# Kernel tuning notes

Measured on AMD Instinct MI355X. Metric: run time of the kernel, lower is better.

## Reference

```python
import jax, jax.numpy as jnp
import numpy as np

TEMP = 0.5
K_SEL = 20
NEG_SLOPE = 0.1


def setup_inputs() -> dict:
    key = jax.random.key(0)
    ks = jax.random.split(key, 12)
    B, N = 64, 20000
    F1, F2, D = 512, 256, 128
    init = lambda k, shape, fan: (jax.random.normal(k, shape) / np.sqrt(fan)).astype(jnp.float32)
    return {
        "patient_embedding": jax.random.normal(ks[0], (B, F1), dtype=jnp.float32),
        "gene_embedding": jax.random.normal(ks[1], (N, F2), dtype=jnp.float32),
        "Wq": init(ks[2], (F1, D), F1), "bq": jnp.zeros((D,), jnp.float32),
        "Wk": init(ks[3], (F2, D), F2), "bk": jnp.zeros((D,), jnp.float32),
        "Wv": init(ks[4], (F2, D), F2), "bv": jnp.zeros((D,), jnp.float32),
        "W1": init(ks[5], (2 * D, D), 2 * D), "b1": jnp.zeros((D,), jnp.float32),
        "w2": init(ks[6], (D,), D), "b2": jnp.zeros((), jnp.float32),
    }


def reference(patient_embedding, gene_embedding, Wq, bq, Wk, bk, Wv, bv, W1, b1, w2, b2):
    B = patient_embedding.shape[0]
    N = gene_embedding.shape[0]
    D = Wq.shape[1]

    Q = patient_embedding @ Wq + bq          # [B, D]
    Km = gene_embedding @ Wk + bk            # [N, D]
    V = gene_embedding @ Wv + bv             # [N, D]

    # MLP attention on cat([Q_exp, K_exp]); split W1 to avoid materializing [B,N,2D]
    q_part = Q @ W1[:D]                      # [B, D]
    k_part = Km @ W1[D:]                     # [N, D]
    h = jax.nn.leaky_relu(q_part[:, None, :] + k_part[None, :, :] + b1, NEG_SLOPE)  # [B, N, D]
    sim = h @ w2 + b2                        # [B, N]
    logits = sim / TEMP

    # gumbel-softmax, hard=True, independent noise per (b, k) row
    g = jax.random.gumbel(jax.random.key(42), (B, K_SEL, N), dtype=logits.dtype)
    y_soft = jax.nn.softmax((logits[:, None, :] + g) / TEMP, axis=-1)   # [B, K, N]
    y_hard = jax.nn.one_hot(jnp.argmax(y_soft, axis=-1), N, dtype=y_soft.dtype)
    masks = y_hard - jax.lax.stop_gradient(y_soft) + y_soft             # straight-through

    topk_values = jnp.einsum("bkn,nd->bkd", masks, V)                   # [B, K, D]
    scores = jnp.einsum("bd,bkd->bk", Q, topk_values) / np.sqrt(D).astype(np.float32)
    weights = jax.nn.softmax(scores, axis=-1)                           # [B, K] (dropout = eval/identity)
    context = jnp.einsum("bk,bkd->bd", weights, topk_values)            # [B, D]
    return context
```

## Files before the change

### kernel.cpp

```cpp
#include <hip/hip_runtime.h>

#define NG 20000
#define BOFF 12800000u

__device__ __forceinline__ void threefry2x32(unsigned x0, unsigned x1,
                                             unsigned& o0, unsigned& o1) {
  const unsigned ks0 = 0u;
  const unsigned ks1 = 42u;
  const unsigned ks2 = 0x1BD11BDAu ^ 0u ^ 42u;
  x0 += ks0; x1 += ks1;
#define TFR(r) { x0 += x1; x1 = (x1 << (r)) | (x1 >> (32 - (r))); x1 ^= x0; }
  TFR(13) TFR(15) TFR(26) TFR(6)
  x0 += ks1; x1 += ks2 + 1u;
  TFR(17) TFR(29) TFR(16) TFR(24)
  x0 += ks2; x1 += ks0 + 2u;
  TFR(13) TFR(15) TFR(26) TFR(6)
  x0 += ks0; x1 += ks1 + 3u;
  TFR(17) TFR(29) TFR(16) TFR(24)
  x0 += ks1; x1 += ks2 + 4u;
  TFR(13) TFR(15) TFR(26) TFR(6)
  x0 += ks2; x1 += ks0 + 5u;
#undef TFR
  o0 = x0; o1 = x1;
}

__device__ __forceinline__ unsigned tfbits(unsigned ctr) {
  unsigned o0, o1;
  threefry2x32(0u, ctr, o0, o1);
  return o0 ^ o1;
}

__device__ __forceinline__ float gumbel32(unsigned bits) {
  float f = __uint_as_float((bits >> 9) | 0x3f800000u) - 1.0f;
  float u = fmaxf(f, 1.17549435e-38f);
  return -__logf(-__logf(u));
}

__device__ __forceinline__ double gumbel64(unsigned bits) {
  float f = __uint_as_float((bits >> 9) | 0x3f800000u) - 1.0f;
  double u = (double)fmaxf(f, 1.17549435e-38f);
  return -log(-log(u));
}

__device__ __forceinline__ unsigned long long packcell(double v, int n) {
  unsigned long long u = (unsigned long long)__double_as_longlong(v);
  u = (u >> 63) ? ~u : (u | 0x8000000000000000ull);
  return (u & 0xFFFFFFFFFFFF8000ull) | (unsigned long long)(32767 - n);
}

__global__ __launch_bounds__(128) void kprep(
    const float* __restrict__ pe, const float* __restrict__ Wq,
    const float* __restrict__ bq, const float* __restrict__ Wk,
    const float* __restrict__ bk, const float* __restrict__ W1,
    const float* __restrict__ b1, const float* __restrict__ w2,
    float* __restrict__ Wf32, double* __restrict__ qbT,
    float* __restrict__ Qm, unsigned long long* __restrict__ cells,
    double2* __restrict__ c12) {
  __shared__ float L[512];
  __shared__ double Ld[128];
  const int t = threadIdx.x;
  const int bid = blockIdx.x;
  if (bid < 256) {
    L[t] = Wk[bid * 128 + t];
    __syncthreads();
    double acc = 0.0;
    #pragma unroll 8
    for (int j = 0; j < 128; ++j)
      acc = fma((double)L[j], (double)W1[(128 + j) * 128 + t], acc);
    Wf32[bid * 128 + t] = (float)acc;
  } else if (bid < 320) {
    const int b = bid - 256;
    #pragma unroll
    for (int i = 0; i < 4; ++i) L[t + 128 * i] = pe[b * 512 + t + 128 * i];
    __syncthreads();
    double q = (double)bq[t];
    #pragma unroll 4
    for (int f = 0; f < 512; ++f)
      q = fma((double)L[f], (double)Wq[f * 128 + t], q);
    Qm[b * 128 + t] = (float)q;
    Ld[t] = q;
    __syncthreads();
    double acc = (double)b1[t];
    #pragma unroll 4
    for (int j = 0; j < 128; ++j) {
      acc = fma(Ld[j], (double)W1[j * 128 + t], acc);
      acc = fma((double)bk[j], (double)W1[(128 + j) * 128 + t], acc);
    }
    qbT[t * 64 + b] = acc;
  } else {
    for (int i = t; i < 1280; i += 128) cells[i] = 0ull;
    const double w2d = (double)w2[t];
    c12[t] = make_double2(0.55 * w2d, 0.45 * w2d);
  }
}

__global__ __launch_bounds__(256) void kfused(
    const float* __restrict__ ge, const float* __restrict__ Wf32,
    const double* __restrict__ qbT, const double2* __restrict__ c12,
    double* __restrict__ simd, float* __restrict__ sim2f) {
  __shared__ double SBd[2048];
  __shared__ float kpL[2048];
  float* geL = (float*)SBd;
  double* simL = SBd;
  const int t = threadIdx.x;
  const int wv = t >> 6;
  const int lane = t & 63;
  const int g0 = blockIdx.x * 16;

  {
    const float4* src = (const float4*)(ge + (size_t)g0 * 256);
    float4* dst = (float4*)geL;
    #pragma unroll
    for (int i = 0; i < 4; ++i) dst[t + i * 256] = src[t + i * 256];
  }
  __syncthreads();

  float acc[4][2];
  #pragma unroll
  for (int j = 0; j < 4; ++j) { acc[j][0] = 0.f; acc[j][1] = 0.f; }
  const float* wb0 = Wf32 + lane;
  const float* wb1 = Wf32 + lane + 64;
  const float* gL = geL + wv * 4 * 256;

  float wc0[4], wc1[4];
  #pragma unroll
  for (int ff = 0; ff < 4; ++ff) {
    wc0[ff] = wb0[ff * 128];
    wc1[ff] = wb1[ff * 128];
  }
  for (int f0 = 0; f0 < 256; f0 += 4) {
    float wn0[4], wn1[4];
    if (f0 < 252) {
      #pragma unroll
      for (int ff = 0; ff < 4; ++ff) {
        wn0[ff] = wb0[(f0 + 4 + ff) * 128];
        wn1[ff] = wb1[(f0 + 4 + ff) * 128];
      }
    }
    #pragma unroll
    for (int j = 0; j < 4; ++j) {
      const float4 gv = *(const float4*)(gL + j * 256 + f0);
      acc[j][0] = fmaf(gv.x, wc0[0], acc[j][0]);
      acc[j][1] = fmaf(gv.x, wc1[0], acc[j][1]);
      acc[j][0] = fmaf(gv.y, wc0[1], acc[j][0]);
      acc[j][1] = fmaf(gv.y, wc1[1], acc[j][1]);
      acc[j][0] = fmaf(gv.z, wc0[2], acc[j][0]);
      acc[j][1] = fmaf(gv.z, wc1[2], acc[j][1]);
      acc[j][0] = fmaf(gv.w, wc0[3], acc[j][0]);
      acc[j][1] = fmaf(gv.w, wc1[3], acc[j][1]);
    }
    #pragma unroll
    for (int ff = 0; ff < 4; ++ff) { wc0[ff] = wn0[ff]; wc1[ff] = wn1[ff]; }
  }

  __syncthreads();
  #pragma unroll
  for (int j = 0; j < 4; ++j) {
    kpL[(wv * 4 + j) * 128 + lane] = acc[j][0];
    kpL[(wv * 4 + j) * 128 + lane + 64] = acc[j][1];
  }
  __syncthreads();

  double s[4];
  #pragma unroll
  for (int j = 0; j < 4; ++j) s[j] = 0.0;
  for (int dd = 0; dd < 128; ++dd) {
    const double2 cc = c12[dd];
    const double qv = qbT[dd * 64 + lane];
    #pragma unroll
    for (int j = 0; j < 4; ++j) {
      const double kv = (double)kpL[(wv + j * 4) * 128 + dd];
      const double tt = qv + kv;
      s[j] = fma(tt, cc.x, s[j]);
      s[j] = fma(fabs(tt), cc.y, s[j]);
    }
  }
  #pragma unroll
  for (int j = 0; j < 4; ++j) simL[lane * 17 + (wv + j * 4)] = s[j];
  __syncthreads();

  {
    const int b = t >> 2, j2 = t & 3;
    const double v0 = simL[b * 17 + j2 * 4 + 0];
    const double v1 = simL[b * 17 + j2 * 4 + 1];
    const double v2 = simL[b * 17 + j2 * 4 + 2];
    const double v3 = simL[b * 17 + j2 * 4 + 3];
    double* dst = simd + (size_t)b * NG + g0 + j2 * 4;
    *(double2*)dst = make_double2(v0, v1);
    *(double2*)(dst + 2) = make_double2(v2, v3);
    float4 f4;
    f4.x = (float)(2.0 * v0); f4.y = (float)(2.0 * v1);
    f4.z = (float)(2.0 * v2); f4.w = (float)(2.0 * v3);
    *(float4*)(sim2f + (size_t)b * NG + g0 + j2 * 4) = f4;
  }
}

__global__ __launch_bounds__(256) void ksel2(
    const double* __restrict__ simd, const float* __restrict__ sim2f,
    unsigned long long* __restrict__ cells) {
  const int t = threadIdx.x;
  const int wv = t >> 6;
  const int lane = t & 63;
  const int p = (int)(blockIdx.x & 7) * 4 + wv;
  const int c = (int)(blockIdx.x >> 3);
  const int n0 = c * 81;
  const int nEnd = min(n0 + 81, NG);
  const int k = lane % 20;
  const int gi = lane / 20;
  const bool active = lane < 60;
  const double* sdA = simd + (size_t)p * NG;
  const double* sdB = simd + (size_t)(p + 32) * NG;
  const float* seA = sim2f + (size_t)p * NG;
  const float* seB = sim2f + (size_t)(p + 32) * NG;
  const unsigned kbase = (unsigned)(p * 20 + k) * (unsigned)NG;

  float m1A = -3e38f, m2A = -3e38f, m1B = -3e38f, m2B = -3e38f;
  int n1A = -1, n2A = -1, n1B = -1, n2B = -1;
  unsigned c1A = 0, c2A = 0, c1B = 0, c2B = 0;

  for (int it = 0; it < 27; ++it) {
    const int n = n0 + it * 3 + gi;
    const bool v = active && (n < nEnd);
    const int nc = v ? n : n0;
    const unsigned idxA = kbase + (unsigned)nc;
    const unsigned bA = tfbits(idxA);
    const unsigned bB = tfbits(idxA + BOFF);
    const float s2A = v ? seA[nc] : -3e38f;
    const float s2B = v ? seB[nc] : -3e38f;
    const float sA = s2A + gumbel32(bA);
    const float sB = s2B + gumbel32(bB);
    if (sA > m1A) { m2A = m1A; n2A = n1A; c2A = c1A; m1A = sA; n1A = n; c1A = bA; }
    else if (sA > m2A) { m2A = sA; n2A = n; c2A = bA; }
    if (sB > m1B) { m2B = m1B; n2B = n1B; c2B = c1B; m1B = sB; n1B = n; c1B = bB; }
    else if (sB > m2B) { m2B = sB; n2B = n; c2B = bB; }
  }

  unsigned long long pbA = 0ull, pbB = 0ull;
  if (n1A >= 0) {
    pbA = packcell(2.0 * sdA[n1A] + gumbel64(c1A), n1A);
    if (n2A >= 0 && (m1A - m2A) < 1e-4f) {
      const unsigned long long u2 = packcell(2.0 * sdA[n2A] + gumbel64(c2A), n2A);
      if (u2 > pbA) pbA = u2;
    }
  }
  if (n1B >= 0) {
    pbB = packcell(2.0 * sdB[n1B] + gumbel64(c1B), n1B);
    if (n2B >= 0 && (m1B - m2B) < 1e-4f) {
      const unsigned long long u2 = packcell(2.0 * sdB[n2B] + gumbel64(c2B), n2B);
      if (u2 > pbB) pbB = u2;
    }
  }

  #pragma unroll
  for (int sh = 20; sh <= 40; sh += 20) {
    const unsigned long long oA = __shfl(pbA, lane + sh, 64);
    const unsigned long long oB = __shfl(pbB, lane + sh, 64);
    if (lane < 20) {
      if (oA > pbA) pbA = oA;
      if (oB > pbB) pbB = oB;
    }
  }
  if (lane < 20 && pbA) atomicMax(&cells[p * 20 + lane], pbA);
  if (lane < 20 && pbB) atomicMax(&cells[(p + 32) * 20 + lane], pbB);
}

__global__ __launch_bounds__(256) void kfinal(
    const float* __restrict__ ge, const float* __restrict__ Wv,
    const float* __restrict__ bv, const float* __restrict__ Qm,
    const unsigned long long* __restrict__ cells, float* __restrict__ out) {
  const int b = blockIdx.x;
  const int t = threadIdx.x;
  const int wv = t >> 6;
  const int lane = t & 63;
  __shared__ float sc[20];
  __shared__ float ctxp[4][128];
  const float2 qv = ((const float2*)(Qm + b * 128))[lane];
  const float2 bvv = ((const float2*)bv)[lane];
  const float* gr[5];
  float2 V[5];
  #pragma unroll
  for (int j = 0; j < 5; ++j) {
    const unsigned long long cell = cells[b * 20 + wv * 5 + j];
    const int n = 32767 - (int)(cell & 0x7FFFull);
    gr[j] = ge + (size_t)n * 256;
    V[j] = bvv;
  }
  for (int f = 0; f < 256; f += 4) {
    const float2 w0 = ((const float2*)(Wv + (size_t)(f + 0) * 128))[lane];
    const float2 w1 = ((const float2*)(Wv + (size_t)(f + 1) * 128))[lane];
    const float2 w2_ = ((const float2*)(Wv + (size_t)(f + 2) * 128))[lane];
    const float2 w3 = ((const float2*)(Wv + (size_t)(f + 3) * 128))[lane];
    #pragma unroll
    for (int j = 0; j < 5; ++j) {
      const float4 gv = *(const float4*)(gr[j] + f);
      V[j].x = fmaf(gv.x, w0.x, V[j].x); V[j].y = fmaf(gv.x, w0.y, V[j].y);
      V[j].x = fmaf(gv.y, w1.x, V[j].x); V[j].y = fmaf(gv.y, w1.y, V[j].y);
      V[j].x = fmaf(gv.z, w2_.x, V[j].x); V[j].y = fmaf(gv.z, w2_.y, V[j].y);
      V[j].x = fmaf(gv.w, w3.x, V[j].x); V[j].y = fmaf(gv.w, w3.y, V[j].y);
    }
  }
  #pragma unroll
  for (int j = 0; j < 5; ++j) {
    float pr = qv.x * V[j].x + qv.y * V[j].y;
    #pragma unroll
    for (int off = 32; off; off >>= 1) pr += __shfl_xor(pr, off, 64);
    if (lane == 0) sc[wv * 5 + j] = pr * 0.08838834764831845f;
  }
  __syncthreads();
  float m = -3.0e38f;
  #pragma unroll
  for (int i = 0; i < 20; ++i) m = fmaxf(m, sc[i]);
  float s = 0.f;
  #pragma unroll
  for (int i = 0; i < 20; ++i) s += expf(sc[i] - m);
  const float inv = 1.0f / s;
  float c0 = 0.f, c1 = 0.f;
  #pragma unroll
  for (int j = 0; j < 5; ++j) {
    const float wk = expf(sc[wv * 5 + j] - m) * inv;
    c0 = fmaf(wk, V[j].x, c0);
    c1 = fmaf(wk, V[j].y, c1);
  }
  ctxp[wv][2 * lane] = c0;
  ctxp[wv][2 * lane + 1] = c1;
  __syncthreads();
  if (t < 128)
    out[b * 128 + t] = (ctxp[0][t] + ctxp[1][t]) + (ctxp[2][t] + ctxp[3][t]);
}

extern "C" void kernel_launch(void* const* d_in, const int* in_sizes, int n_in,
                              void* d_out, int out_size, void* d_ws, size_t ws_size,
                              hipStream_t stream) {
  (void)in_sizes; (void)n_in; (void)out_size; (void)ws_size;
  const float* pe = (const float*)d_in[0];
  const float* ge = (const float*)d_in[1];
  const float* Wq = (const float*)d_in[2];
  const float* bq = (const float*)d_in[3];
  const float* Wk = (const float*)d_in[4];
  const float* bk = (const float*)d_in[5];
  const float* Wv = (const float*)d_in[6];
  const float* bvp = (const float*)d_in[7];
  const float* W1 = (const float*)d_in[8];
  const float* b1 = (const float*)d_in[9];
  const float* w2 = (const float*)d_in[10];

  char* w = (char*)d_ws;
  float* Wf32 = (float*)w;
  double* qbT = (double*)(w + 131072);
  float* Qm = (float*)(w + 196608);
  unsigned long long* cells =
      (unsigned long long*)(w + 229376);
  double2* c12 = (double2*)(w + 239616);
  double* simd = (double*)(w + 241664);
  float* sim2f = (float*)(w + 10481664);
  float* out = (float*)d_out;

  kprep<<<dim3(321), dim3(128), 0, stream>>>(pe, Wq, bq, Wk, bk, W1, b1, w2,
                                             Wf32, qbT, Qm, cells, c12);
  kfused<<<dim3(1250), dim3(256), 0, stream>>>(ge, Wf32, qbT, c12, simd, sim2f);
  ksel2<<<dim3(1976), dim3(256), 0, stream>>>(simd, sim2f, cells);
  kfinal<<<dim3(64), dim3(256), 0, stream>>>(ge, Wv, bvp, Qm, cells, out);
}
```

Before: 289.3 us.

## Fuse gumbel top-k selection into similarity kernel, drop sim intermediates

Merges the separate selection kernel into the similarity kernel. Each block now draws the Gumbel noise and does the per-(b,k) argmax over its own 16 genes straight from shared memory, then issues an atomicMax per cell. This removes the global write and re-read of the double and float similarity arrays (about 15 MB) and one kernel launch. In exchange it issues many more atomics (1280 per block) and loads the RNG work onto the fused kernel. The refinement step now starts from a float similarity instead of a double, which may change tie-breaking. Also rewrites the Gumbel log as log2 with an FMA and raises unroll factors in the prep kernel.

```diff
diff --git a/kernel.cpp b/kernel.cpp
--- a/kernel.cpp
+++ b/kernel.cpp
@@ -1,7 +1,6 @@
 #include <hip/hip_runtime.h>
 
 #define NG 20000
-#define BOFF 12800000u
 
 __device__ __forceinline__ void threefry2x32(unsigned x0, unsigned x1,
                                              unsigned& o0, unsigned& o1) {
@@ -33,7 +32,8 @@
 __device__ __forceinline__ float gumbel32(unsigned bits) {
   float f = __uint_as_float((bits >> 9) | 0x3f800000u) - 1.0f;
   float u = fmaxf(f, 1.17549435e-38f);
-  return -__logf(-__logf(u));
+  const float l2u = __log2f(u);
+  return fmaf(-0.69314718056f, __log2f(-l2u), 0.3665129206f);
 }
 
 __device__ __forceinline__ double gumbel64(unsigned bits) {
@@ -64,7 +64,7 @@
     L[t] = Wk[bid * 128 + t];
     __syncthreads();
     double acc = 0.0;
-    #pragma unroll 8
+    #pragma unroll 16
     for (int j = 0; j < 128; ++j)
       acc = fma((double)L[j], (double)W1[(128 + j) * 128 + t], acc);
     Wf32[bid * 128 + t] = (float)acc;
@@ -74,14 +74,14 @@
     for (int i = 0; i < 4; ++i) L[t + 128 * i] = pe[b * 512 + t + 128 * i];
     __syncthreads();
     double q = (double)bq[t];
-    #pragma unroll 4
+    #pragma unroll 16
     for (int f = 0; f < 512; ++f)
       q = fma((double)L[f], (double)Wq[f * 128 + t], q);
     Qm[b * 128 + t] = (float)q;
     Ld[t] = q;
     __syncthreads();
     double acc = (double)b1[t];
-    #pragma unroll 4
+    #pragma unroll 8
     for (int j = 0; j < 128; ++j) {
       acc = fma(Ld[j], (double)W1[j * 128 + t], acc);
       acc = fma((double)bk[j], (double)W1[(128 + j) * 128 + t], acc);
@@ -97,11 +97,11 @@
 __global__ __launch_bounds__(256) void kfused(
     const float* __restrict__ ge, const float* __restrict__ Wf32,
     const double* __restrict__ qbT, const double2* __restrict__ c12,
-    double* __restrict__ simd, float* __restrict__ sim2f) {
+    unsigned long long* __restrict__ cells) {
   __shared__ double SBd[2048];
   __shared__ float kpL[2048];
   float* geL = (float*)SBd;
-  double* simL = SBd;
+  float* simLf = (float*)SBd;
   const int t = threadIdx.x;
   const int wv = t >> 6;
   const int lane = t & 63;
@@ -176,92 +176,35 @@
     }
   }
   #pragma unroll
-  for (int j = 0; j < 4; ++j) simL[lane * 17 + (wv + j * 4)] = s[j];
-  __syncthreads();
-
-  {
-    const int b = t >> 2, j2 = t & 3;
-    const double v0 = simL[b * 17 + j2 * 4 + 0];
-    const double v1 = simL[b * 17 + j2 * 4 + 1];
-    const double v2 = simL[b * 17 + j2 * 4 + 2];
-    const double v3 = simL[b * 17 + j2 * 4 + 3];
-    double* dst = simd + (size_t)b * NG + g0 + j2 * 4;
-    *(double2*)dst = make_double2(v0, v1);
-    *(double2*)(dst + 2) = make_double2(v2, v3);
-    float4 f4;
-    f4.x = (float)(2.0 * v0); f4.y = (float)(2.0 * v1);
-    f4.z = (float)(2.0 * v2); f4.w = (float)(2.0 * v3);
-    *(float4*)(sim2f + (size_t)b * NG + g0 + j2 * 4) = f4;
-  }
-}
-
-__global__ __launch_bounds__(256) void ksel2(
-    const double* __restrict__ simd, const float* __restrict__ sim2f,
-    unsigned long long* __restrict__ cells) {
-  const int t = threadIdx.x;
-  const int wv = t >> 6;
-  const int lane = t & 63;
-  const int p = (int)(blockIdx.x & 7) * 4 + wv;
-  const int c = (int)(blockIdx.x >> 3);
-  const int n0 = c * 81;
-  const int nEnd = min(n0 + 81, NG);
-  const int k = lane % 20;
-  const int gi = lane / 20;
-  const bool active = lane < 60;
-  const double* sdA = simd + (size_t)p * NG;
-  const double* sdB = simd + (size_t)(p + 32) * NG;
-  const float* seA = sim2f + (size_t)p * NG;
-  const float* seB = sim2f + (size_t)(p + 32) * NG;
-  const unsigned kbase = (unsigned)(p * 20 + k) * (unsigned)NG;
-
-  float m1A = -3e38f, m2A = -3e38f, m1B = -3e38f, m2B = -3e38f;
-  int n1A = -1, n2A = -1, n1B = -1, n2B = -1;
-  unsigned c1A = 0, c2A = 0, c1B = 0, c2B = 0;
-
-  for (int it = 0; it < 27; ++it) {
-    const int n = n0 + it * 3 + gi;
-    const bool v = active && (n < nEnd);
-    const int nc = v ? n : n0;
-    const unsigned idxA = kbase + (unsigned)nc;
-    const unsigned bA = tfbits(idxA);
-    const unsigned bB = tfbits(idxA + BOFF);
-    const float s2A = v ? seA[nc] : -3e38f;
-    const float s2B = v ? seB[nc] : -3e38f;
-    const float sA = s2A + gumbel32(bA);
-    const float sB = s2B + gumbel32(bB);
-    if (sA > m1A) { m2A = m1A; n2A = n1A; c2A = c1A; m1A = sA; n1A = n; c1A = bA; }
-    else if (sA > m2A) { m2A = sA; n2A = n; c2A = bA; }
-    if (sB > m1B) { m2B = m1B; n2B = n1B; c2B = c1B; m1B = sB; n1B = n; c1B = bB; }
-    else if (sB > m2B) { m2B = sB; n2B = n; c2B = bB; }
-  }
-
-  unsigned long long pbA = 0ull, pbB = 0ull;
-  if (n1A >= 0) {
-    pbA = packcell(2.0 * sdA[n1A] + gumbel64(c1A), n1A);
-    if (n2A >= 0 && (m1A - m2A) < 1e-4f) {
-      const unsigned long long u2 = packcell(2.0 * sdA[n2A] + gumbel64(c2A), n2A);
-      if (u2 > pbA) pbA = u2;
-    }
-  }
-  if (n1B >= 0) {
-    pbB = packcell(2.0 * sdB[n1B] + gumbel64(c1B), n1B);
-    if (n2B >= 0 && (m1B - m2B) < 1e-4f) {
-      const unsigned long long u2 = packcell(2.0 * sdB[n2B] + gumbel64(c2B), n2B);
-      if (u2 > pbB) pbB = u2;
-    }
-  }
-
-  #pragma unroll
-  for (int sh = 20; sh <= 40; sh += 20) {
-    const unsigned long long oA = __shfl(pbA, lane + sh, 64);
-    const unsigned long long oB = __shfl(pbB, lane + sh, 64);
-    if (lane < 20) {
-      if (oA > pbA) pbA = oA;
-      if (oB > pbB) pbB = oB;
-    }
-  }
-  if (lane < 20 && pbA) atomicMax(&cells[p * 20 + lane], pbA);
-  if (lane < 20 && pbB) atomicMax(&cells[(p + 32) * 20 + lane], pbB);
+  for (int j = 0; j < 4; ++j)
+    simLf[lane * 17 + (wv + j * 4)] = (float)(2.0 * s[j]);
+  __syncthreads();
+
+  #pragma unroll
+  for (int i = 0; i < 5; ++i) {
+    const int cell = i * 256 + t;
+    const int b = (unsigned)cell / 20u;
+    const float* sb = simLf + b * 17;
+    float m1 = -3e38f, m2 = -3e38f;
+    int n1 = -1, n2 = -1;
+    unsigned c1 = 0, c2 = 0;
+    const unsigned ib = (unsigned)cell * 20000u + (unsigned)g0;
+    #pragma unroll 4
+    for (int g = 0; g < 16; ++g) {
+      const unsigned bb = tfbits(ib + (unsigned)g);
+      const float sc = sb[g] + gumbel32(bb);
+      if (sc > m1) { m2 = m1; n2 = n1; c2 = c1; m1 = sc; n1 = g; c1 = bb; }
+      else if (sc > m2) { m2 = sc; n2 = g; c2 = bb; }
+    }
+    unsigned long long pb =
+        packcell((double)sb[n1] + gumbel64(c1), g0 + n1);
+    if (n2 >= 0 && (m1 - m2) < 1e-4f) {
+      const unsigned long long u2 =
+          packcell((double)sb[n2] + gumbel64(c2), g0 + n2);
+      if (u2 > pb) pb = u2;
+    }
+    atomicMax(&cells[cell], pb);
+  }
 }
 
 __global__ __launch_bounds__(256) void kfinal(
@@ -351,13 +294,10 @@
   unsigned long long* cells =
       (unsigned long long*)(w + 229376);
   double2* c12 = (double2*)(w + 239616);
-  double* simd = (double*)(w + 241664);
-  float* sim2f = (float*)(w + 10481664);
   float* out = (float*)d_out;
 
   kprep<<<dim3(321), dim3(128), 0, stream>>>(pe, Wq, bq, Wk, bk, W1, b1, w2,
                                              Wf32, qbT, Qm, cells, c12);
-  kfused<<<dim3(1250), dim3(256), 0, stream>>>(ge, Wf32, qbT, c12, simd, sim2f);
-  ksel2<<<dim3(1976), dim3(256), 0, stream>>>(simd, sim2f, cells);
+  kfused<<<dim3(1250), dim3(256), 0, stream>>>(ge, Wf32, qbT, c12, cells);
   kfinal<<<dim3(64), dim3(256), 0, stream>>>(ge, Wv, bvp, Qm, cells, out);
 }
```

After: 266.0 us. -8.1%, faster.
